# Optimization experiments

Measured on AMD Instinct MI355X. Metric: run time of the kernel, lower is better.

The kernel has to match this reference:

```python
import jax, jax.numpy as jnp
import numpy as np

LOSS_ALPHA = 0.7  # Config.loss_alpha


def setup_inputs() -> dict:
    key = jax.random.key(0)
    k1, k2, k3 = jax.random.split(key, 3)
    N, D, K = 1024, 256, 65536
    online_emb = jax.random.normal(k1, (N, D), dtype=jnp.float32)
    mom_emb = jax.random.normal(k2, (N, D), dtype=jnp.float32)
    queue = jax.random.normal(k3, (D, K), dtype=jnp.float32)
    temp = jnp.full((1,), 0.07, dtype=jnp.float32)
    return {"online_emb": online_emb, "mom_emb": mom_emb, "queue": queue, "temp": temp}


def _ce_label0(logits):
    # cross-entropy with target class 0 for every row, mean over batch
    return jnp.mean(jax.nn.logsumexp(logits, axis=1) - logits[:, 0])


def reference(online_emb, mom_emb, queue, temp):
    pos_sim = jnp.einsum('nd,nd->n', online_emb, mom_emb)          # [N]
    neg_sim = jnp.einsum('nd,dk->nk', online_emb, queue)           # [N, K]
    logits_raw = jnp.concatenate([pos_sim[:, None], neg_sim], axis=1)  # [N, K+1]
    t = temp[0]
    loss_online = _ce_label0(logits_raw / t)
    loss_momentum = _ce_label0(logits_raw / jax.lax.stop_gradient(t))
    return LOSS_ALPHA * loss_online + (1.0 - LOSS_ALPHA) * loss_momentum
```

## Files before the change

### kernel.cpp

```cpp
#include <hip/hip_runtime.h>
#include <hip/hip_bf16.h>


#define NROWS 1024
#define DDIM  256
#define KQ    65536
#define BN    128
#define NPART 512
#define LN2_F 0.69314718055994531f

typedef short  short8  __attribute__((ext_vector_type(8)));
typedef float  floatx4 __attribute__((ext_vector_type(4)));

__device__ __forceinline__ unsigned short f2bf(float f) {
    unsigned int u = __float_as_uint(f);
    u += 0x7FFFu + ((u >> 16) & 1u);
    return (unsigned short)(u >> 16);
}

__global__ __launch_bounds__(256)
void conv_a(const float* __restrict__ A, const float* __restrict__ mom,
            const float* __restrict__ temp,
            unsigned short* __restrict__ Ab, float* __restrict__ pos2)
{
    const float s = 1.0f / (temp[0] * LN2_F);
    const int i = blockIdx.x * 256 + threadIdx.x;
    const floatx4 v = ((const floatx4*)A)[i];
    ushort4 w;
    w.x = f2bf(v.x * s); w.y = f2bf(v.y * s);
    w.z = f2bf(v.z * s); w.w = f2bf(v.w * s);
    ((ushort4*)Ab)[i] = w;

    const floatx4 m = ((const floatx4*)mom)[i];
    float d = v.x * m.x + v.y * m.y + v.z * m.z + v.w * m.w;
    d += __shfl_xor(d, 1, 64);
    d += __shfl_xor(d, 2, 64);
    d += __shfl_xor(d, 4, 64);
    d += __shfl_xor(d, 8, 64);
    d += __shfl_xor(d, 16, 64);
    d += __shfl_xor(d, 32, 64);
    if ((threadIdx.x & 63) == 0)
        pos2[i >> 6] = d * s;
}

__global__ __launch_bounds__(256, 2)
void gemm_softmax(const unsigned short* __restrict__ Ab,
                  const float* __restrict__ Q,
                  float2* __restrict__ partials)
{
    __shared__ __align__(16) unsigned short Bl[BN * DDIM];

    const int tid  = threadIdx.x;
    const int lane = tid & 63;
    const int wave = tid >> 6;
    const int l15  = lane & 15;
    const int quad = lane >> 4;
    const int nb   = blockIdx.x;
    const int nbase = nb * BN;

    #pragma unroll
    for (int iter = 0; iter < 4; ++iter) {
        const int t2 = iter * 256 + tid;
        const int ny = t2 & 31;
        const int ko = t2 >> 5;
        floatx4 v[8];
        #pragma unroll
        for (int j = 0; j < 8; ++j)
            v[j] = __builtin_nontemporal_load(
                       (const floatx4*)(Q + (size_t)(ko * 8 + j) * KQ + nbase + ny * 4));
        #pragma unroll
        for (int i2 = 0; i2 < 4; ++i2) {
            const int n = ny * 4 + i2;
            const int phys = ko ^ (n & 15);
            short8 w;
            #pragma unroll
            for (int j = 0; j < 8; ++j)
                w[j] = (short)f2bf(v[j][i2]);
            *(short8*)&Bl[n * DDIM + phys * 8] = w;
        }
    }
    __syncthreads();

    #pragma unroll 1
    for (int g = 0; g < 4; ++g) {
        const int rowbase = g * 256 + wave * 64;
        const unsigned short* apb = Ab + (size_t)(rowbase + l15) * DDIM + quad * 8;

        floatx4 acc[4][8] = {};
        short8 af[4];
        #pragma unroll
        for (int i = 0; i < 4; ++i)
            af[i] = *(const short8*)(apb + i * 16 * DDIM);

        #pragma unroll 1
        for (int s = 0; s < 8; ++s) {
            const int sn = (s + 1) & 7;
            short8 afn[4];
            #pragma unroll
            for (int i = 0; i < 4; ++i)
                afn[i] = *(const short8*)(apb + i * 16 * DDIM + sn * 32);

            const int vb = l15 * 512 + (((4 * s + quad) ^ l15) * 16);
            short8 bfv[8];
            #pragma unroll
            for (int j = 0; j < 8; ++j)
                bfv[j] = *(const short8*)((const char*)Bl + vb + j * 8192);

            #pragma unroll
            for (int i = 0; i < 4; ++i)
                #pragma unroll
                for (int j = 0; j < 8; ++j)
                    acc[i][j] = __builtin_amdgcn_mfma_f32_16x16x32_bf16(af[i], bfv[j], acc[i][j], 0, 0, 0);

            #pragma unroll
            for (int i = 0; i < 4; ++i) af[i] = afn[i];
        }

        #pragma unroll
        for (int i = 0; i < 4; ++i) {
            float2 tmp[4];
            #pragma unroll
            for (int r = 0; r < 4; ++r) {
                float mx = acc[i][0][r];
                #pragma unroll
                for (int j = 1; j < 8; ++j) mx = fmaxf(mx, acc[i][j][r]);
                mx = fmaxf(mx, __shfl_xor(mx, 1, 64));
                mx = fmaxf(mx, __shfl_xor(mx, 2, 64));
                mx = fmaxf(mx, __shfl_xor(mx, 4, 64));
                mx = fmaxf(mx, __shfl_xor(mx, 8, 64));
                float s2 = 0.f;
                #pragma unroll
                for (int j = 0; j < 8; ++j)
                    s2 += __builtin_amdgcn_exp2f(acc[i][j][r] - mx);
                s2 += __shfl_xor(s2, 1, 64);
                s2 += __shfl_xor(s2, 2, 64);
                s2 += __shfl_xor(s2, 4, 64);
                s2 += __shfl_xor(s2, 8, 64);
                tmp[r] = make_float2(mx, s2);
            }
            if (l15 == 0) {
                const int row = rowbase + i * 16 + quad * 4;
                floatx4* dst = (floatx4*)(partials + (size_t)nb * NROWS + row);
                floatx4 w0 = {tmp[0].x, tmp[0].y, tmp[1].x, tmp[1].y};
                floatx4 w1 = {tmp[2].x, tmp[2].y, tmp[3].x, tmp[3].y};
                __builtin_nontemporal_store(w0, dst);
                __builtin_nontemporal_store(w1, dst + 1);
            }
        }
    }
}

__global__ __launch_bounds__(256)
void finalize_rows(const float2* __restrict__ partials,
                   const float* __restrict__ pos2,
                   float* __restrict__ out)
{
    const int t   = threadIdx.x;
    const int rl  = t & 15;
    const int grp = t >> 4;
    const int row = blockIdx.x * 16 + rl;

    float M = -3.0e38f, S = 0.f;
    #pragma unroll 1
    for (int pb = 0; pb < 32; pb += 8) {
        float2 v[8];
        #pragma unroll
        for (int j = 0; j < 8; ++j)
            v[j] = partials[(size_t)(grp * 32 + pb + j) * NROWS + row];
        #pragma unroll
        for (int j = 0; j < 8; ++j) {
            const float M2 = fmaxf(M, v[j].x);
            S = S * __builtin_amdgcn_exp2f(M - M2) + v[j].y * __builtin_amdgcn_exp2f(v[j].x - M2);
            M = M2;
        }
    }

    __shared__ float2 sm[16][17];
    sm[grp][rl] = make_float2(M, S);
    __syncthreads();

    if (t < 64) {
        float val = 0.f;
        if (t < 16) {
            float Mm = -3.0e38f, Ss = 0.f;
            #pragma unroll
            for (int g2 = 0; g2 < 16; ++g2) {
                const float2 v = sm[g2][t];
                const float M2 = fmaxf(Mm, v.x);
                Ss = Ss * __builtin_amdgcn_exp2f(Mm - M2) + v.y * __builtin_amdgcn_exp2f(v.x - M2);
                Mm = M2;
            }
            const float p  = pos2[blockIdx.x * 16 + t];
            const float M2 = fmaxf(Mm, p);
            const float L  = Ss * __builtin_amdgcn_exp2f(Mm - M2) + __builtin_amdgcn_exp2f(p - M2);
            val = (M2 + __builtin_amdgcn_logf(L) - p) * LN2_F;
        }
        val += __shfl_xor(val, 1, 64);
        val += __shfl_xor(val, 2, 64);
        val += __shfl_xor(val, 4, 64);
        val += __shfl_xor(val, 8, 64);
        val += __shfl_xor(val, 16, 64);
        val += __shfl_xor(val, 32, 64);
        if (t == 0) atomicAdd(out, val * (1.0f / (float)NROWS));
    }
}

extern "C" void kernel_launch(void* const* d_in, const int* in_sizes, int n_in,
                              void* d_out, int out_size, void* d_ws, size_t ws_size,
                              hipStream_t stream)
{
    const float* online = (const float*)d_in[0];
    const float* mom    = (const float*)d_in[1];
    const float* queue  = (const float*)d_in[2];
    const float* temp   = (const float*)d_in[3];
    float* out = (float*)d_out;

    char* ws = (char*)d_ws;
    unsigned short* Ab = (unsigned short*)ws;
    float2* partials   = (float2*)(ws + 524288);
    float*  pos2       = (float*)(ws + 524288 + 4194304);

    (void)hipMemsetAsync(out, 0, sizeof(float), stream);
    conv_a<<<256, 256, 0, stream>>>(online, mom, temp, Ab, pos2);
    gemm_softmax<<<KQ / BN, 256, 0, stream>>>(Ab, queue, partials);
    finalize_rows<<<64, 256, 0, stream>>>(partials, pos2, out);
}
```

Measured before the change: 158.2 us.

## Double-buffer GEMM fragments, use DPP reductions, move pos-sim to finalize, drop memset

The GEMM inner loop now ping-pongs two register sets for the A and B fragments, so the loads for the next k-step are issued before the current MFMAs run. The 16-lane max and sum reductions use DPP moves instead of shuffles. The positive-similarity dot product moves from conv_a into finalize_rows, and the output memset is replaced by a zero write in conv_a, which removes one launch and a workspace buffer. The double buffer raises register pressure under launch_bounds(256,2), and the zero write relies on conv_a finishing before finalize_rows runs its atomics.

Result: faster. 150.9 us (-4.6%).

```diff
diff --git a/kernel.cpp b/kernel.cpp
--- a/kernel.cpp
+++ b/kernel.cpp
@@ -18,11 +18,29 @@
     return (unsigned short)(u >> 16);
 }
 
+#define DPPMOV(x, ctrl) \
+    __uint_as_float(__builtin_amdgcn_mov_dpp(__float_as_uint(x), (ctrl), 0xF, 0xF, true))
+
+__device__ __forceinline__ float dpp16_max(float x) {
+    x = fmaxf(x, DPPMOV(x, 0xB1));
+    x = fmaxf(x, DPPMOV(x, 0x4E));
+    x = fmaxf(x, DPPMOV(x, 0x141));
+    x = fmaxf(x, DPPMOV(x, 0x140));
+    return x;
+}
+__device__ __forceinline__ float dpp16_sum(float x) {
+    x += DPPMOV(x, 0xB1);
+    x += DPPMOV(x, 0x4E);
+    x += DPPMOV(x, 0x141);
+    x += DPPMOV(x, 0x140);
+    return x;
+}
+
 __global__ __launch_bounds__(256)
-void conv_a(const float* __restrict__ A, const float* __restrict__ mom,
-            const float* __restrict__ temp,
-            unsigned short* __restrict__ Ab, float* __restrict__ pos2)
-{
+void conv_a(const float* __restrict__ A, const float* __restrict__ temp,
+            unsigned short* __restrict__ Ab, float* __restrict__ out)
+{
+    if (blockIdx.x == 0 && threadIdx.x == 0) out[0] = 0.0f;
     const float s = 1.0f / (temp[0] * LN2_F);
     const int i = blockIdx.x * 256 + threadIdx.x;
     const floatx4 v = ((const floatx4*)A)[i];
@@ -30,17 +48,6 @@
     w.x = f2bf(v.x * s); w.y = f2bf(v.y * s);
     w.z = f2bf(v.z * s); w.w = f2bf(v.w * s);
     ((ushort4*)Ab)[i] = w;
-
-    const floatx4 m = ((const floatx4*)mom)[i];
-    float d = v.x * m.x + v.y * m.y + v.z * m.z + v.w * m.w;
-    d += __shfl_xor(d, 1, 64);
-    d += __shfl_xor(d, 2, 64);
-    d += __shfl_xor(d, 4, 64);
-    d += __shfl_xor(d, 8, 64);
-    d += __shfl_xor(d, 16, 64);
-    d += __shfl_xor(d, 32, 64);
-    if ((threadIdx.x & 63) == 0)
-        pos2[i >> 6] = d * s;
 }
 
 __global__ __launch_bounds__(256, 2)
@@ -87,33 +94,51 @@
         const unsigned short* apb = Ab + (size_t)(rowbase + l15) * DDIM + quad * 8;
 
         floatx4 acc[4][8] = {};
-        short8 af[4];
+        short8 afA[4], afB[4], bfA[8], bfB[8];
+
         #pragma unroll
         for (int i = 0; i < 4; ++i)
-            af[i] = *(const short8*)(apb + i * 16 * DDIM);
+            afA[i] = *(const short8*)(apb + i * 16 * DDIM);
+        {
+            const int vb = l15 * 512 + ((quad ^ l15) * 16);
+            #pragma unroll
+            for (int j = 0; j < 8; ++j)
+                bfA[j] = *(const short8*)((const char*)Bl + vb + j * 8192);
+        }
 
         #pragma unroll 1
-        for (int s = 0; s < 8; ++s) {
-            const int sn = (s + 1) & 7;
-            short8 afn[4];
-            #pragma unroll
-            for (int i = 0; i < 4; ++i)
-                afn[i] = *(const short8*)(apb + i * 16 * DDIM + sn * 32);
-
-            const int vb = l15 * 512 + (((4 * s + quad) ^ l15) * 16);
-            short8 bfv[8];
-            #pragma unroll
-            for (int j = 0; j < 8; ++j)
-                bfv[j] = *(const short8*)((const char*)Bl + vb + j * 8192);
-
-            #pragma unroll
-            for (int i = 0; i < 4; ++i)
-                #pragma unroll
-                for (int j = 0; j < 8; ++j)
-                    acc[i][j] = __builtin_amdgcn_mfma_f32_16x16x32_bf16(af[i], bfv[j], acc[i][j], 0, 0, 0);
-
-            #pragma unroll
-            for (int i = 0; i < 4; ++i) af[i] = afn[i];
+        for (int sp = 0; sp < 4; ++sp) {
+            const int s1 = 2 * sp + 1;
+            #pragma unroll
+            for (int i = 0; i < 4; ++i)
+                afB[i] = *(const short8*)(apb + i * 16 * DDIM + s1 * 32);
+            {
+                const int vb = l15 * 512 + (((4 * s1 + quad) ^ l15) * 16);
+                #pragma unroll
+                for (int j = 0; j < 8; ++j)
+                    bfB[j] = *(const short8*)((const char*)Bl + vb + j * 8192);
+            }
+            #pragma unroll
+            for (int i = 0; i < 4; ++i)
+                #pragma unroll
+                for (int j = 0; j < 8; ++j)
+                    acc[i][j] = __builtin_amdgcn_mfma_f32_16x16x32_bf16(afA[i], bfA[j], acc[i][j], 0, 0, 0);
+
+            const int s2 = (2 * sp + 2) & 7;
+            #pragma unroll
+            for (int i = 0; i < 4; ++i)
+                afA[i] = *(const short8*)(apb + i * 16 * DDIM + s2 * 32);
+            {
+                const int vb = l15 * 512 + (((4 * s2 + quad) ^ l15) * 16);
+                #pragma unroll
+                for (int j = 0; j < 8; ++j)
+                    bfA[j] = *(const short8*)((const char*)Bl + vb + j * 8192);
+            }
+            #pragma unroll
+            for (int i = 0; i < 4; ++i)
+                #pragma unroll
+                for (int j = 0; j < 8; ++j)
+                    acc[i][j] = __builtin_amdgcn_mfma_f32_16x16x32_bf16(afB[i], bfB[j], acc[i][j], 0, 0, 0);
         }
 
         #pragma unroll
@@ -124,18 +149,12 @@
                 float mx = acc[i][0][r];
                 #pragma unroll
                 for (int j = 1; j < 8; ++j) mx = fmaxf(mx, acc[i][j][r]);
-                mx = fmaxf(mx, __shfl_xor(mx, 1, 64));
-                mx = fmaxf(mx, __shfl_xor(mx, 2, 64));
-                mx = fmaxf(mx, __shfl_xor(mx, 4, 64));
-                mx = fmaxf(mx, __shfl_xor(mx, 8, 64));
+                mx = dpp16_max(mx);
                 float s2 = 0.f;
                 #pragma unroll
                 for (int j = 0; j < 8; ++j)
                     s2 += __builtin_amdgcn_exp2f(acc[i][j][r] - mx);
-                s2 += __shfl_xor(s2, 1, 64);
-                s2 += __shfl_xor(s2, 2, 64);
-                s2 += __shfl_xor(s2, 4, 64);
-                s2 += __shfl_xor(s2, 8, 64);
+                s2 = dpp16_sum(s2);
                 tmp[r] = make_float2(mx, s2);
             }
             if (l15 == 0) {
@@ -152,10 +171,31 @@
 
 __global__ __launch_bounds__(256)
 void finalize_rows(const float2* __restrict__ partials,
-                   const float* __restrict__ pos2,
+                   const float* __restrict__ online,
+                   const float* __restrict__ mom,
+                   const float* __restrict__ temp,
                    float* __restrict__ out)
 {
-    const int t   = threadIdx.x;
+    const int t = threadIdx.x;
+    __shared__ float2 sm[16][17];
+    __shared__ float sm_pos[16];
+
+    {
+        const float s = 1.0f / (temp[0] * LN2_F);
+        const int r2 = t >> 4, c2 = t & 15;
+        const float* po = online + (size_t)(blockIdx.x * 16 + r2) * DDIM + c2 * 16;
+        const float* pm = mom    + (size_t)(blockIdx.x * 16 + r2) * DDIM + c2 * 16;
+        float d = 0.f;
+        #pragma unroll
+        for (int w = 0; w < 4; ++w) {
+            const floatx4 a = *(const floatx4*)(po + w * 4);
+            const floatx4 b = *(const floatx4*)(pm + w * 4);
+            d += a.x * b.x + a.y * b.y + a.z * b.z + a.w * b.w;
+        }
+        d = dpp16_sum(d);
+        if (c2 == 0) sm_pos[r2] = d * s;
+    }
+
     const int rl  = t & 15;
     const int grp = t >> 4;
     const int row = blockIdx.x * 16 + rl;
@@ -174,8 +214,6 @@
             M = M2;
         }
     }
-
-    __shared__ float2 sm[16][17];
     sm[grp][rl] = make_float2(M, S);
     __syncthreads();
 
@@ -190,7 +228,7 @@
                 Ss = Ss * __builtin_amdgcn_exp2f(Mm - M2) + v.y * __builtin_amdgcn_exp2f(v.x - M2);
                 Mm = M2;
             }
-            const float p  = pos2[blockIdx.x * 16 + t];
+            const float p  = sm_pos[t];
             const float M2 = fmaxf(Mm, p);
             const float L  = Ss * __builtin_amdgcn_exp2f(Mm - M2) + __builtin_amdgcn_exp2f(p - M2);
             val = (M2 + __builtin_amdgcn_logf(L) - p) * LN2_F;
@@ -218,10 +256,8 @@
     char* ws = (char*)d_ws;
     unsigned short* Ab = (unsigned short*)ws;
     float2* partials   = (float2*)(ws + 524288);
-    float*  pos2       = (float*)(ws + 524288 + 4194304);
-
-    (void)hipMemsetAsync(out, 0, sizeof(float), stream);
-    conv_a<<<256, 256, 0, stream>>>(online, mom, temp, Ab, pos2);
+
+    conv_a<<<256, 256, 0, stream>>>(online, temp, Ab, out);
     gemm_softmax<<<KQ / BN, 256, 0, stream>>>(Ab, queue, partials);
-    finalize_rows<<<64, 256, 0, stream>>>(partials, pos2, out);
-}
+    finalize_rows<<<64, 256, 0, stream>>>(partials, online, mom, temp, out);
+}
```
